# Kernel tuning notes

Hardware: AMD Instinct MI355X
Metric: run time of the kernel (lower is better)

Reference implementation:

```python
import jax, jax.numpy as jnp
import numpy as np

D_MODEL = 1024
N_HEADS = 16
HEAD = D_MODEL // N_HEADS
B, T = 4, 2048


def setup_inputs() -> dict:
    key = jax.random.key(0)
    ks = jax.random.split(key, 8)
    s = 0.02
    return {
        "x_enc": jax.random.normal(ks[0], (B, T, D_MODEL), dtype=jnp.float32),
        "x_dec": jax.random.normal(ks[1], (B, T, D_MODEL), dtype=jnp.float32),
        "mask": jnp.zeros((B, T, T), dtype=jnp.float32),
        "Wq": jax.random.normal(ks[2], (D_MODEL, D_MODEL), dtype=jnp.float32) * s,
        "bq": jnp.zeros((D_MODEL,), dtype=jnp.float32),
        "Wkv": jax.random.normal(ks[3], (D_MODEL, 2 * D_MODEL), dtype=jnp.float32) * s,
        "bkv": jnp.zeros((2 * D_MODEL,), dtype=jnp.float32),
        "Wo": jax.random.normal(ks[4], (D_MODEL, D_MODEL), dtype=jnp.float32) * s,
        "bo": jnp.zeros((D_MODEL,), dtype=jnp.float32),
    }


def reference(x_enc, x_dec, mask, Wq, bq, Wkv, bkv, Wo, bo):
    b, t, c = x_enc.shape
    # projections
    kv = x_enc @ Wkv + bkv                     # [B,T,2C]
    q = x_dec @ Wq + bq                        # [B,T,C]
    # split heads (replicates torch reshape of interleaved kv)
    kv = kv.reshape(b, t, N_HEADS, 2 * HEAD).transpose(0, 2, 1, 3)  # [B,H,T,2hs]
    q = q.reshape(b, t, N_HEADS, HEAD).transpose(0, 2, 1, 3)        # [B,H,T,hs]
    k, v = kv[..., :HEAD], kv[..., HEAD:]
    # attention
    scores = jnp.einsum("bhqd,bhkd->bhqk", q, k) / np.sqrt(HEAD).astype(np.float32)
    scores = scores + mask[:, None, :, :]      # additive mask, broadcast over heads
    attn = jax.nn.softmax(scores, axis=-1)
    res = jnp.einsum("bhqk,bhkd->bhqd", attn, v)   # [B,H,T,hs]
    res = res.transpose(0, 2, 1, 3).reshape(b, t, c)
    return res @ Wo + bo
```

## Files before the change

kernel.cpp:

```cpp
#include <hip/hip_runtime.h>
#include <hip/hip_bf16.h>


#define D_MODEL 1024
#define NH      16
#define HEAD    64
#define BATCH   4
#define SEQ     2048
#define QB      128

typedef unsigned int   u32;
typedef unsigned short u16;
typedef __attribute__((ext_vector_type(8))) short s16x8;
typedef __attribute__((ext_vector_type(4))) float f32x4;

__device__ __forceinline__ u16 tobf(float f) {
    u32 u = __builtin_bit_cast(u32, f);
    return (u16)((u + 0x7fffu + ((u >> 16) & 1u)) >> 16);
}
__device__ __forceinline__ float frombf(u16 u) {
    return __builtin_bit_cast(float, (u32)u << 16);
}
__device__ __forceinline__ u32 pack_bf2(float a, float b) {
    return (u32)tobf(a) | ((u32)tobf(b) << 16);
}

__device__ __forceinline__ void gl_lds16(const void* g, void* l) {
    __builtin_amdgcn_global_load_lds(
        (const __attribute__((address_space(1))) u32*)g,
        (__attribute__((address_space(3))) u32*)l, 16, 0, 0);
}

__global__ __launch_bounds__(256) void cast_bf16(
    const float* __restrict__ in, u16* __restrict__ out, int n)
{
    int i = (blockIdx.x * 256 + threadIdx.x) * 4;
    if (i < n) {
        float4 v = *(const float4*)(in + i);
        ushort4 o = make_ushort4(tobf(v.x), tobf(v.y), tobf(v.z), tobf(v.w));
        *(ushort4*)(out + i) = o;
    }
}

__global__ __launch_bounds__(256) void mask_prep(
    const float* __restrict__ mask, u16* __restrict__ mp)
{
    const size_t gt = (size_t)blockIdx.x * 256 + threadIdx.x;
    const int l = (int)(gt & 63);
    const size_t tile = gt >> 6;
    const int kt = (int)(tile & 127);
    const size_t bq = tile >> 7;
    const int qt = (int)(bq & 127);
    const int b  = (int)(bq >> 7);
    const int q15 = l & 15, quad = l >> 4;
    const int q = qt*16 + q15;
    const int k = kt*16 + quad*4;
    float4 v = *(const float4*)&mask[((size_t)(b*SEQ + q))*SEQ + k];
    ushort4 o = make_ushort4(tobf(v.x), tobf(v.y), tobf(v.z), tobf(v.w));
    *(ushort4*)&mp[tile*256 + (size_t)l*4] = o;
}

__global__ __launch_bounds__(256) void transpose_cast(
    const float* __restrict__ W, u16* __restrict__ WT, int K, int N)
{
    __shared__ __align__(16) float tile[32][33];
    const int n0 = blockIdx.x * 32, k0 = blockIdx.y * 32;
    const int r = threadIdx.x >> 3, c4 = (threadIdx.x & 7) * 4;
    float4 v = *(const float4*)&W[(size_t)(k0 + r) * N + n0 + c4];
    tile[r][c4] = v.x; tile[r][c4+1] = v.y; tile[r][c4+2] = v.z; tile[r][c4+3] = v.w;
    __syncthreads();
    ushort4 o = make_ushort4(tobf(tile[c4+0][r]), tobf(tile[c4+1][r]),
                             tobf(tile[c4+2][r]), tobf(tile[c4+3][r]));
    *(ushort4*)&WT[(size_t)(n0 + r) * K + k0 + c4] = o;
}

__device__ __forceinline__ void store_out(u16* p, float v)  { *p = tobf(v); }
__device__ __forceinline__ void store_out(float* p, float v){ *p = v; }

template <typename OT>
__global__ __launch_bounds__(256) void gemm_bt(
    const u16* __restrict__ A, const u16* __restrict__ Bt,
    const float* __restrict__ bias, OT* __restrict__ C,
    int N, int K, float out_scale)
{
    __shared__ __align__(16) u16 As[128 * 32];
    __shared__ __align__(16) u16 Bs[128 * 32];
    const int t = threadIdx.x;
    const int w = t >> 6, l = t & 63;
    const int lane15 = l & 15, quad = l >> 4;
    const int m0 = blockIdx.y * 128, n0 = blockIdx.x * 128;
    const int wm = (w >> 1) * 64, wn = (w & 1) * 64;
    const int lr = l >> 2, lk = (l & 3) * 8;

    f32x4 acc[4][4] = {};

    for (int k0 = 0; k0 < K; k0 += 32) {
        __syncthreads();
        #pragma unroll
        for (int i = 0; i < 2; ++i) {
            const int chunk = w * 2 + i;
            gl_lds16(A  + (size_t)(m0 + chunk*16 + lr) * K + k0 + lk,
                     As + chunk * 512);
            gl_lds16(Bt + (size_t)(n0 + chunk*16 + lr) * K + k0 + lk,
                     Bs + chunk * 512);
        }
        __syncthreads();
        s16x8 af[4], bfr[4];
        #pragma unroll
        for (int i = 0; i < 4; ++i)
            af[i] = *(const s16x8*)&As[(wm + i*16 + lane15) * 32 + quad * 8];
        #pragma unroll
        for (int j = 0; j < 4; ++j)
            bfr[j] = *(const s16x8*)&Bs[(wn + j*16 + lane15) * 32 + quad * 8];
        #pragma unroll
        for (int i = 0; i < 4; ++i)
            #pragma unroll
            for (int j = 0; j < 4; ++j)
                acc[i][j] = __builtin_amdgcn_mfma_f32_16x16x32_bf16(
                    af[i], bfr[j], acc[i][j], 0, 0, 0);
    }
    #pragma unroll
    for (int j = 0; j < 4; ++j) {
        const int col = n0 + wn + j*16 + lane15;
        const float bv = bias[col];
        #pragma unroll
        for (int i = 0; i < 4; ++i)
            #pragma unroll
            for (int r = 0; r < 4; ++r) {
                const int row = m0 + wm + i*16 + quad*4 + r;
                store_out(C + (size_t)row * N + col, (acc[i][j][r] + bv) * out_scale);
            }
    }
}

__global__ __launch_bounds__(256) void v_transpose(
    const u16* __restrict__ kvb, u16* __restrict__ vt)
{
    __shared__ __align__(16) u16 tile[64][72];
    const int t  = threadIdx.x;
    const int t0 = blockIdx.x * 64;
    const int bh = blockIdx.y;
    const int b = bh >> 4, h = bh & 15;
    const int r = t >> 2, c = (t & 3) * 16;
    const u16* g = kvb + (size_t)(b*SEQ + t0 + r) * (2*D_MODEL) + h*128 + 64 + c;
    *(uint4*)&tile[r][c]     = *(const uint4*)g;
    *(uint4*)&tile[r][c + 8] = *(const uint4*)(g + 8);
    __syncthreads();
    u16 buf[16];
    #pragma unroll
    for (int i = 0; i < 16; ++i) buf[i] = tile[c + i][r];
    u16* o = vt + (size_t)(bh*64 + r) * SEQ + t0 + c;
    *(uint4*)o       = *(uint4*)&buf[0];
    *(uint4*)(o + 8) = *(uint4*)&buf[8];
}

__global__ __launch_bounds__(256, 3) void attn_mfma(
    const u16* __restrict__ qb, const u16* __restrict__ kvb,
    const u16* __restrict__ vt, const u16* __restrict__ mp,
    u16* __restrict__ resb)
{
    __shared__ __align__(16) u16 sm[4*4096 + 4*32*72];
    const int t = threadIdx.x;
    const int w = t >> 6, l = t & 63;
    const int lane15 = l & 15, quad = l >> 4;
    const int h  = blockIdx.x;
    const int q0 = blockIdx.y * QB;
    const int b  = blockIdx.z;
    const int bh = b * NH + h;
    const int lr4 = l >> 2, lc8 = (l & 3) * 8;

    s16x8 aq0[2], aq1[2];
    #pragma unroll
    for (int s = 0; s < 2; ++s) {
        const u16* qrow = qb + (size_t)(b*SEQ + q0 + w*32 + s*16 + lane15) * D_MODEL + h*HEAD;
        aq0[s] = *(const s16x8*)(qrow + quad*8);
        aq1[s] = *(const s16x8*)(qrow + 32 + quad*8);
    }
    const u16* mrow[2];
    #pragma unroll
    for (int s = 0; s < 2; ++s)
        mrow[s] = mp + (((size_t)b*128 + (q0>>4) + w*2 + s) * 128) * 256 + (size_t)l*4;

    auto stage = [&](int k0s, int bf) {
        #pragma unroll
        for (int i = 0; i < 2; ++i) {
            const int c = w*2 + i;
            const int hh = c & 1, rr = c >> 1;
            const u16* kg = kvb + (size_t)(b*SEQ + k0s + rr*16 + lr4) * (2*D_MODEL)
                                + h*128 + hh*32 + lc8;
            gl_lds16(kg, sm + bf*4096 + hh*2048 + rr*512);
            const u16* vg = vt + (size_t)(bh*64 + rr*16 + lr4) * SEQ
                               + k0s + hh*32 + lc8;
            gl_lds16(vg, sm + 8192 + bf*4096 + hh*2048 + rr*512);
        }
    };

    f32x4 o_acc[2][4] = {};
    float l_i[2] = {0.f, 0.f};
    ushort4 mreg[2][4];

    stage(0, 0);
    #pragma unroll
    for (int s = 0; s < 2; ++s)
        #pragma unroll
        for (int nt = 0; nt < 4; ++nt)
            mreg[s][nt] = *(const ushort4*)(mrow[s] + (size_t)nt * 256);

    u16* const Ps = sm + 16384;

    for (int it = 0; it < SEQ/64; ++it) {
        const int k0 = it * 64;
        const int bf = it & 1;
        __syncthreads();
        ushort4 mnxt[2][4];
        if (it + 1 < SEQ/64) {
            stage(k0 + 64, bf ^ 1);
            #pragma unroll
            for (int s = 0; s < 2; ++s)
                #pragma unroll
                for (int nt = 0; nt < 4; ++nt)
                    mnxt[s][nt] = *(const ushort4*)(mrow[s] + ((size_t)((k0+64)>>4) + nt) * 256);
        }

        s16x8 kf[4][2];
        #pragma unroll
        for (int nt = 0; nt < 4; ++nt) {
            kf[nt][0] = *(const s16x8*)(sm + bf*4096 +        (nt*16 + lane15)*32 + quad*8);
            kf[nt][1] = *(const s16x8*)(sm + bf*4096 + 2048 + (nt*16 + lane15)*32 + quad*8);
        }

        #pragma unroll
        for (int s = 0; s < 2; ++s) {
            f32x4 sv[4];
            #pragma unroll
            for (int nt = 0; nt < 4; ++nt) {
                sv[nt][0] = frombf(mreg[s][nt].x); sv[nt][1] = frombf(mreg[s][nt].y);
                sv[nt][2] = frombf(mreg[s][nt].z); sv[nt][3] = frombf(mreg[s][nt].w);
                sv[nt] = __builtin_amdgcn_mfma_f32_16x16x32_bf16(kf[nt][0], aq0[s], sv[nt], 0, 0, 0);
                sv[nt] = __builtin_amdgcn_mfma_f32_16x16x32_bf16(kf[nt][1], aq1[s], sv[nt], 0, 0, 0);
            }
            float rs = 0.f;
            #pragma unroll
            for (int nt = 0; nt < 4; ++nt)
                #pragma unroll
                for (int r = 0; r < 4; ++r) {
                    float p = __expf(sv[nt][r]);
                    sv[nt][r] = p;
                    rs += p;
                }
            rs += __shfl_xor(rs, 16);
            rs += __shfl_xor(rs, 32);
            l_i[s] += rs;
            u16* prow = Ps + (w*32 + s*16 + lane15) * 72;
            #pragma unroll
            for (int nt = 0; nt < 4; ++nt) {
                uint2 pv = make_uint2(pack_bf2(sv[nt][0], sv[nt][1]),
                                      pack_bf2(sv[nt][2], sv[nt][3]));
                *(uint2*)&prow[nt*16 + quad*4] = pv;
            }
        }

        #pragma unroll
        for (int s = 0; s < 2; ++s) {
            const u16* prow = Ps + (w*32 + s*16 + lane15) * 72;
            s16x8 pf0 = *(const s16x8*)&prow[quad*8];
            s16x8 pf1 = *(const s16x8*)&prow[32 + quad*8];
            #pragma unroll
            for (int dt = 0; dt < 4; ++dt) {
                s16x8 vf0 = *(const s16x8*)(sm + 8192 + bf*4096 +        (dt*16 + lane15)*32 + quad*8);
                s16x8 vf1 = *(const s16x8*)(sm + 8192 + bf*4096 + 2048 + (dt*16 + lane15)*32 + quad*8);
                o_acc[s][dt] = __builtin_amdgcn_mfma_f32_16x16x32_bf16(vf0, pf0, o_acc[s][dt], 0, 0, 0);
                o_acc[s][dt] = __builtin_amdgcn_mfma_f32_16x16x32_bf16(vf1, pf1, o_acc[s][dt], 0, 0, 0);
            }
        }

        if (it + 1 < SEQ/64) {
            #pragma unroll
            for (int s = 0; s < 2; ++s)
                #pragma unroll
                for (int nt = 0; nt < 4; ++nt)
                    mreg[s][nt] = mnxt[s][nt];
        }
    }

    __syncthreads();
    #pragma unroll
    for (int s = 0; s < 2; ++s) {
        const float inv = 1.f / l_i[s];
        u16* orow = &sm[(w*32 + s*16 + lane15) * 72];
        #pragma unroll
        for (int dt = 0; dt < 4; ++dt) {
            uint2 ov = make_uint2(pack_bf2(o_acc[s][dt][0]*inv, o_acc[s][dt][1]*inv),
                                  pack_bf2(o_acc[s][dt][2]*inv, o_acc[s][dt][3]*inv));
            *(uint2*)&orow[dt*16 + quad*4] = ov;
        }
    }
    __syncthreads();
    {
        const int tr = t >> 1, tc = (t & 1) * 32;
        u16* o = resb + (size_t)(b*SEQ + q0 + tr) * D_MODEL + h*HEAD + tc;
        #pragma unroll
        for (int j = 0; j < 4; ++j)
            *(uint4*)(o + j*8) = *(const uint4*)&sm[tr*72 + tc + j*8];
    }
}

extern "C" void kernel_launch(void* const* d_in, const int* in_sizes, int n_in,
                              void* d_out, int out_size, void* d_ws, size_t ws_size,
                              hipStream_t stream) {
    const float* x_enc = (const float*)d_in[0];
    const float* x_dec = (const float*)d_in[1];
    const float* mask  = (const float*)d_in[2];
    const float* Wq    = (const float*)d_in[3];
    const float* bq    = (const float*)d_in[4];
    const float* Wkv   = (const float*)d_in[5];
    const float* bkv   = (const float*)d_in[6];
    const float* Wo    = (const float*)d_in[7];
    const float* bo    = (const float*)d_in[8];
    float* out = (float*)d_out;

    const int M = BATCH * SEQ;
    u16* xe   = (u16*)d_ws;
    u16* xd   = xe   + (size_t)M * D_MODEL;
    u16* wqT  = xd   + (size_t)M * D_MODEL;
    u16* wkvT = wqT  + (size_t)D_MODEL * D_MODEL;
    u16* woT  = wkvT + (size_t)2*D_MODEL*D_MODEL;
    u16* qbuf = woT  + (size_t)D_MODEL * D_MODEL;
    u16* kvb  = qbuf + (size_t)M * D_MODEL;
    u16* vtb  = kvb  + (size_t)M * 2 * D_MODEL;
    u16* resb = vtb  + (size_t)BATCH*NH*HEAD*SEQ;
    u16* mpk  = xe;

    const int NX = M * D_MODEL;
    cast_bf16<<<NX/1024, 256, 0, stream>>>(x_enc, xe, NX);
    cast_bf16<<<NX/1024, 256, 0, stream>>>(x_dec, xd, NX);
    transpose_cast<<<dim3(D_MODEL/32, D_MODEL/32), 256, 0, stream>>>(Wq,  wqT,  D_MODEL, D_MODEL);
    transpose_cast<<<dim3(2*D_MODEL/32, D_MODEL/32), 256, 0, stream>>>(Wkv, wkvT, D_MODEL, 2*D_MODEL);
    transpose_cast<<<dim3(D_MODEL/32, D_MODEL/32), 256, 0, stream>>>(Wo,  woT,  D_MODEL, D_MODEL);

    gemm_bt<u16><<<dim3(2*D_MODEL/128, M/128), 256, 0, stream>>>(
        xe, wkvT, bkv, kvb, 2*D_MODEL, D_MODEL, 1.0f);
    gemm_bt<u16><<<dim3(D_MODEL/128, M/128), 256, 0, stream>>>(
        xd, wqT, bq, qbuf, D_MODEL, D_MODEL, 0.125f);
    mask_prep<<<(BATCH*128*128*64)/256, 256, 0, stream>>>(mask, mpk);
    v_transpose<<<dim3(SEQ/64, BATCH*NH), 256, 0, stream>>>(kvb, vtb);
    attn_mfma<<<dim3(NH, SEQ/QB, BATCH), 256, 0, stream>>>(
        qbuf, kvb, vtb, mpk, resb);
    gemm_bt<float><<<dim3(D_MODEL/128, M/128), 256, 0, stream>>>(
        resb, woT, bo, out, D_MODEL, D_MODEL, 1.0f);
}
```

Baseline: 436.4 us.

## Fold log2e into Q scale and mask, sum softmax rows via MFMA, swizzle LDS

```diff
diff --git a/kernel.cpp b/kernel.cpp
--- a/kernel.cpp
+++ b/kernel.cpp
@@ -1,5 +1,6 @@
 #include <hip/hip_runtime.h>
 #include <hip/hip_bf16.h>
+#include <math.h>
 
 
 #define D_MODEL 1024
@@ -9,6 +10,8 @@
 #define SEQ     2048
 #define QB      128
 
+#define LOG2E   1.44269504088896f
+
 typedef unsigned int   u32;
 typedef unsigned short u16;
 typedef __attribute__((ext_vector_type(8))) short s16x8;
@@ -21,8 +24,10 @@
 __device__ __forceinline__ float frombf(u16 u) {
     return __builtin_bit_cast(float, (u32)u << 16);
 }
-__device__ __forceinline__ u32 pack_bf2(float a, float b) {
-    return (u32)tobf(a) | ((u32)tobf(b) << 16);
+__device__ __forceinline__ u32 cvtpk(float a, float b) {
+    u32 r;
+    asm("v_cvt_pk_bf16_f32 %0, %1, %2" : "=v"(r) : "v"(a), "v"(b));
+    return r;
 }
 
 __device__ __forceinline__ void gl_lds16(const void* g, void* l) {
@@ -56,7 +61,8 @@
     const int q = qt*16 + q15;
     const int k = kt*16 + quad*4;
     float4 v = *(const float4*)&mask[((size_t)(b*SEQ + q))*SEQ + k];
-    ushort4 o = make_ushort4(tobf(v.x), tobf(v.y), tobf(v.z), tobf(v.w));
+    ushort4 o = make_ushort4(tobf(v.x * LOG2E), tobf(v.y * LOG2E),
+                             tobf(v.z * LOG2E), tobf(v.w * LOG2E));
     *(ushort4*)&mp[tile*256 + (size_t)l*4] = o;
 }
 
@@ -167,7 +173,9 @@
     const int q0 = blockIdx.y * QB;
     const int b  = blockIdx.z;
     const int bh = b * NH + h;
-    const int lr4 = l >> 2, lc8 = (l & 3) * 8;
+    const int lr4 = l >> 2;
+    const int lc8 = (((l & 3) ^ (lr4 & 3)) * 8);
+    const int cq  = (quad ^ (lane15 & 3)) * 8;
 
     s16x8 aq0[2], aq1[2];
     #pragma unroll
@@ -196,8 +204,11 @@
     };
 
     f32x4 o_acc[2][4] = {};
-    float l_i[2] = {0.f, 0.f};
+    f32x4 l_acc[2] = {};
     ushort4 mreg[2][4];
+    s16x8 vones;
+    #pragma unroll
+    for (int i = 0; i < 8; ++i) vones[i] = (short)0x3F80;
 
     stage(0, 0);
     #pragma unroll
@@ -225,8 +236,8 @@
         s16x8 kf[4][2];
         #pragma unroll
         for (int nt = 0; nt < 4; ++nt) {
-            kf[nt][0] = *(const s16x8*)(sm + bf*4096 +        (nt*16 + lane15)*32 + quad*8);
-            kf[nt][1] = *(const s16x8*)(sm + bf*4096 + 2048 + (nt*16 + lane15)*32 + quad*8);
+            kf[nt][0] = *(const s16x8*)(sm + bf*4096 +        (nt*16 + lane15)*32 + cq);
+            kf[nt][1] = *(const s16x8*)(sm + bf*4096 + 2048 + (nt*16 + lane15)*32 + cq);
         }
 
         #pragma unroll
@@ -236,43 +247,47 @@
             for (int nt = 0; nt < 4; ++nt) {
                 sv[nt][0] = frombf(mreg[s][nt].x); sv[nt][1] = frombf(mreg[s][nt].y);
                 sv[nt][2] = frombf(mreg[s][nt].z); sv[nt][3] = frombf(mreg[s][nt].w);
+            }
+            __builtin_amdgcn_s_setprio(1);
+            #pragma unroll
+            for (int nt = 0; nt < 4; ++nt) {
                 sv[nt] = __builtin_amdgcn_mfma_f32_16x16x32_bf16(kf[nt][0], aq0[s], sv[nt], 0, 0, 0);
                 sv[nt] = __builtin_amdgcn_mfma_f32_16x16x32_bf16(kf[nt][1], aq1[s], sv[nt], 0, 0, 0);
             }
-            float rs = 0.f;
-            #pragma unroll
-            for (int nt = 0; nt < 4; ++nt)
-                #pragma unroll
-                for (int r = 0; r < 4; ++r) {
-                    float p = __expf(sv[nt][r]);
-                    sv[nt][r] = p;
-                    rs += p;
-                }
-            rs += __shfl_xor(rs, 16);
-            rs += __shfl_xor(rs, 32);
-            l_i[s] += rs;
+            __builtin_amdgcn_s_setprio(0);
             u16* prow = Ps + (w*32 + s*16 + lane15) * 72;
             #pragma unroll
             for (int nt = 0; nt < 4; ++nt) {
-                uint2 pv = make_uint2(pack_bf2(sv[nt][0], sv[nt][1]),
-                                      pack_bf2(sv[nt][2], sv[nt][3]));
-                *(uint2*)&prow[nt*16 + quad*4] = pv;
-            }
-        }
-
+                float p0 = exp2f(sv[nt][0]), p1 = exp2f(sv[nt][1]);
+                float p2 = exp2f(sv[nt][2]), p3 = exp2f(sv[nt][3]);
+                *(uint2*)&prow[nt*16 + quad*4] = make_uint2(cvtpk(p0, p1), cvtpk(p2, p3));
+            }
+        }
+
+        s16x8 pf[2][2];
         #pragma unroll
         for (int s = 0; s < 2; ++s) {
             const u16* prow = Ps + (w*32 + s*16 + lane15) * 72;
-            s16x8 pf0 = *(const s16x8*)&prow[quad*8];
-            s16x8 pf1 = *(const s16x8*)&prow[32 + quad*8];
-            #pragma unroll
-            for (int dt = 0; dt < 4; ++dt) {
-                s16x8 vf0 = *(const s16x8*)(sm + 8192 + bf*4096 +        (dt*16 + lane15)*32 + quad*8);
-                s16x8 vf1 = *(const s16x8*)(sm + 8192 + bf*4096 + 2048 + (dt*16 + lane15)*32 + quad*8);
-                o_acc[s][dt] = __builtin_amdgcn_mfma_f32_16x16x32_bf16(vf0, pf0, o_acc[s][dt], 0, 0, 0);
-                o_acc[s][dt] = __builtin_amdgcn_mfma_f32_16x16x32_bf16(vf1, pf1, o_acc[s][dt], 0, 0, 0);
-            }
-        }
+            pf[s][0] = *(const s16x8*)&prow[quad*8];
+            pf[s][1] = *(const s16x8*)&prow[32 + quad*8];
+        }
+        __builtin_amdgcn_s_setprio(1);
+        #pragma unroll
+        for (int s = 0; s < 2; ++s) {
+            l_acc[s] = __builtin_amdgcn_mfma_f32_16x16x32_bf16(vones, pf[s][0], l_acc[s], 0, 0, 0);
+            l_acc[s] = __builtin_amdgcn_mfma_f32_16x16x32_bf16(vones, pf[s][1], l_acc[s], 0, 0, 0);
+        }
+        #pragma unroll
+        for (int dt = 0; dt < 4; ++dt) {
+            s16x8 vf0 = *(const s16x8*)(sm + 8192 + bf*4096 +        (dt*16 + lane15)*32 + cq);
+            s16x8 vf1 = *(const s16x8*)(sm + 8192 + bf*4096 + 2048 + (dt*16 + lane15)*32 + cq);
+            #pragma unroll
+            for (int s = 0; s < 2; ++s) {
+                o_acc[s][dt] = __builtin_amdgcn_mfma_f32_16x16x32_bf16(vf0, pf[s][0], o_acc[s][dt], 0, 0, 0);
+                o_acc[s][dt] = __builtin_amdgcn_mfma_f32_16x16x32_bf16(vf1, pf[s][1], o_acc[s][dt], 0, 0, 0);
+            }
+        }
+        __builtin_amdgcn_s_setprio(0);
 
         if (it + 1 < SEQ/64) {
             #pragma unroll
@@ -286,13 +301,13 @@
     __syncthreads();
     #pragma unroll
     for (int s = 0; s < 2; ++s) {
-        const float inv = 1.f / l_i[s];
+        const float inv = 1.f / l_acc[s][0];
         u16* orow = &sm[(w*32 + s*16 + lane15) * 72];
         #pragma unroll
         for (int dt = 0; dt < 4; ++dt) {
-            uint2 ov = make_uint2(pack_bf2(o_acc[s][dt][0]*inv, o_acc[s][dt][1]*inv),
-                                  pack_bf2(o_acc[s][dt][2]*inv, o_acc[s][dt][3]*inv));
-            *(uint2*)&orow[dt*16 + quad*4] = ov;
+            *(uint2*)&orow[dt*16 + quad*4] = make_uint2(
+                cvtpk(o_acc[s][dt][0]*inv, o_acc[s][dt][1]*inv),
+                cvtpk(o_acc[s][dt][2]*inv, o_acc[s][dt][3]*inv));
         }
     }
     __syncthreads();
@@ -341,7 +356,7 @@
     gemm_bt<u16><<<dim3(2*D_MODEL/128, M/128), 256, 0, stream>>>(
         xe, wkvT, bkv, kvb, 2*D_MODEL, D_MODEL, 1.0f);
     gemm_bt<u16><<<dim3(D_MODEL/128, M/128), 256, 0, stream>>>(
-        xd, wqT, bq, qbuf, D_MODEL, D_MODEL, 0.125f);
+        xd, wqT, bq, qbuf, D_MODEL, D_MODEL, 0.125f * LOG2E);
     mask_prep<<<(BATCH*128*128*64)/256, 256, 0, stream>>>(mask, mpk);
     v_transpose<<<dim3(SEQ/64, BATCH*NH), 256, 0, stream>>>(kvb, vtb);
     attn_mfma<<<dim3(NH, SEQ/QB, BATCH), 256, 0, stream>>>(
```

Result: no change. 437.0 us (+0.1%).
